# Kernel tuning notes

Measured on AMD Instinct MI355X. Metric: run time of the kernel, lower is better.

Reference implementation:

```python
import jax, jax.numpy as jnp
import numpy as np

B, L, N, D, C, WS, NH = 32, 64, 1024, 512, 8192, 3, 16
HD = D // NH          # head_dim = 32
HID = 2 * D           # MLP expansion = 2


def _ln(x, g, b, eps=1e-5):
    m = jnp.mean(x, -1, keepdims=True)
    v = jnp.mean((x - m) ** 2, -1, keepdims=True)
    return (x - m) * jax.lax.rsqrt(v + eps) * g + b


def setup_inputs() -> dict:
    key = jax.random.key(0)
    ks = jax.random.split(key, 16)
    r = lambda i, shape, s=0.02: jax.random.normal(ks[i], shape, jnp.float32) * s
    return dict(
        visual_features=jax.random.normal(ks[0], (B, N, D), jnp.float32),
        targets=jax.random.randint(ks[1], (B, L), 0, C),
        pad_id=1,
        char_embed=r(2, (C, D), 1.0),
        ln1_g=jnp.ones(D), ln1_b=jnp.zeros(D),
        in_proj_w=r(3, (3 * D, D)), in_proj_b=jnp.zeros(3 * D),
        out_w=r(4, (D, D)), out_b=jnp.zeros(D),
        fc1_w=r(5, (HID, D)), fc1_b=jnp.zeros(HID),
        fc2_w=r(6, (D, HID)), fc2_b=jnp.zeros(D),
        ln2_g=jnp.ones(D), ln2_b=jnp.zeros(D),
        left_token=r(7, (1, 1, D)), right_token=r(8, (1, 1, D)),
        q_w=r(9, (D, D)), q_b=jnp.zeros(D),
        kv_w=r(10, (2 * D, D)), kv_b=jnp.zeros(2 * D),
        proj_w=r(11, (D, D)), proj_b=jnp.zeros(D),
        lnq_g=jnp.ones(D), lnq_b=jnp.zeros(D),
        lnkv_g=jnp.ones(D), lnkv_b=jnp.zeros(D),
        head_w=r(12, (C, D)), head_b=jnp.zeros(C),
    )


def reference(visual_features, targets, pad_id, char_embed, ln1_g, ln1_b,
              in_proj_w, in_proj_b, out_w, out_b, fc1_w, fc1_b, fc2_w, fc2_b,
              ln2_g, ln2_b, left_token, right_token, q_w, q_b, kv_w, kv_b,
              proj_w, proj_b, lnq_g, lnq_b, lnkv_g, lnkv_b, head_w, head_b):
    # --- build left/right context windows via gather (vectorizes the python loop) ---
    padded = jnp.pad(targets, ((0, 0), (WS, WS)), constant_values=pad_id)
    li = jnp.arange(L)[:, None] + jnp.arange(WS)[None, :]      # (L, WS)
    left_ids = padded[:, li]                                   # (B, L, WS)
    right_ids = padded[:, li + WS + 1]                         # (B, L, WS)

    def encode(ids, tok):
        x = char_embed[ids] + tok                 # (B, L, WS, D)
        x = x.reshape(B * L, WS, D)               # (M, WS, D)
        xn = _ln(x, ln1_g, ln1_b)
        qkv = xn @ in_proj_w.T + in_proj_b
        q, k, v = jnp.split(qkv, 3, -1)
        sh = lambda t: t.reshape(B * L, WS, NH, HD).transpose(0, 2, 1, 3)
        q, k, v = sh(q), sh(k), sh(v)
        a = jax.nn.softmax(jnp.einsum('mhqd,mhkd->mhqk', q, k) * HD ** -0.5, -1)
        o = jnp.einsum('mhqk,mhkd->mhqd', a, v).transpose(0, 2, 1, 3).reshape(B * L, WS, D)
        x = x + o @ out_w.T + out_b
        h = jax.nn.gelu(_ln(x, ln2_g, ln2_b) @ fc1_w.T + fc1_b, approximate=False)
        x = x + h @ fc2_w.T + fc2_b
        return x.mean(1).reshape(B, L, D)

    def cross(qs):
        q = _ln(qs, lnq_g, lnq_b) @ q_w.T + q_b
        kv = _ln(visual_features, lnkv_g, lnkv_b) @ kv_w.T + kv_b
        k, v = jnp.split(kv, 2, -1)
        q = q.reshape(B, L, NH, HD).transpose(0, 2, 1, 3)
        k = k.reshape(B, N, NH, HD).transpose(0, 2, 1, 3)
        v = v.reshape(B, N, NH, HD).transpose(0, 2, 1, 3)
        a = jax.nn.softmax(jnp.einsum('bhld,bhnd->bhln', q, k) * HD ** -0.5, -1)
        o = jnp.einsum('bhln,bhnd->bhld', a, v).transpose(0, 2, 1, 3).reshape(B, L, D)
        return o @ proj_w.T + proj_b

    left_enc = encode(left_ids, left_token)
    right_enc = encode(right_ids, right_token)
    left_feat = left_enc + cross(left_enc)
    right_feat = right_enc + cross(right_enc)
    sgm_left = left_feat @ head_w.T + head_b      # (B, L, C)
    sgm_right = right_feat @ head_w.T + head_b    # (B, L, C)
    return sgm_left, sgm_right, targets
```

## Files before the change

### kernel.cpp

```cpp
#include <hip/hip_runtime.h>
#include <hip/hip_bf16.h>
#include <cstdint>
#include <cstddef>


typedef __attribute__((ext_vector_type(8))) short s16x8;
typedef __attribute__((ext_vector_type(8))) unsigned short u16x8;
typedef __attribute__((ext_vector_type(4))) unsigned short u16x4;
typedef __attribute__((ext_vector_type(4))) float f32x4;

__device__ __forceinline__ float b2f(unsigned short u) {
  union { unsigned int i; float f; } c; c.i = ((unsigned int)u) << 16; return c.f;
}
__device__ __forceinline__ unsigned short f2b(float f) {
  union { float f; unsigned int i; } c; c.f = f;
  unsigned int x = c.i;
  return (unsigned short)((x + 0x7FFFu + ((x >> 16) & 1u)) >> 16);
}

#define GLOAD16(gp, lp)                                                        \
  __builtin_amdgcn_global_load_lds(                                           \
      (const __attribute__((address_space(1))) void*)(gp),                    \
      (__attribute__((address_space(3))) void*)(lp), 16, 0, 0)

__global__ void cvt_f32_bf16(const float* __restrict__ s, unsigned short* __restrict__ d, int n4) {
  int i = blockIdx.x * 256 + threadIdx.x;
  if (i >= n4) return;
  float4 v = ((const float4*)s)[i];
  u16x4 o; o[0] = f2b(v.x); o[1] = f2b(v.y); o[2] = f2b(v.z); o[3] = f2b(v.w);
  *(u16x4*)(d + (size_t)i * 4) = o;
}

__global__ void embed_k(const int* __restrict__ targets, const int* __restrict__ pad_p,
                        const float* __restrict__ ce, const float* __restrict__ ltok,
                        const float* __restrict__ rtok, float* __restrict__ x) {
  int idx = blockIdx.x * 256 + threadIdx.x;
  if (idx >= 12288 * 128) return;
  int row = idx >> 7, d4 = idx & 127;
  int side = row >= 6144;
  int rem = row - side * 6144;
  int pos = rem / 3, w = rem - pos * 3;
  int b = pos >> 6, l = pos & 63;
  int id;
  if (!side) { int ti = l + w - 3; id = (ti >= 0) ? targets[(b << 6) + ti] : *pad_p; }
  else       { int ti = l + w + 1; id = (ti < 64) ? targets[(b << 6) + ti] : *pad_p; }
  float4 cv = ((const float4*)ce)[(size_t)id * 128 + d4];
  float4 tv = ((const float4*)(side ? rtok : ltok))[d4];
  float4 o; o.x = cv.x + tv.x; o.y = cv.y + tv.y; o.z = cv.z + tv.z; o.w = cv.w + tv.w;
  ((float4*)x)[idx] = o;
}

__global__ __launch_bounds__(256) void ln_rows(const float* __restrict__ in,
    const float* __restrict__ g, const float* __restrict__ b,
    unsigned short* __restrict__ out, int M) {
  int row = blockIdx.x * 4 + (threadIdx.x >> 6);
  int lane = threadIdx.x & 63;
  const float* rp = in + (size_t)row * 512;
  float4 v0 = ((const float4*)rp)[lane * 2];
  float4 v1 = ((const float4*)rp)[lane * 2 + 1];
  float vv[8] = {v0.x, v0.y, v0.z, v0.w, v1.x, v1.y, v1.z, v1.w};
  float s = 0.f, ss = 0.f;
#pragma unroll
  for (int j = 0; j < 8; ++j) { s += vv[j]; ss += vv[j] * vv[j]; }
#pragma unroll
  for (int o = 1; o < 64; o <<= 1) { s += __shfl_xor(s, o); ss += __shfl_xor(ss, o); }
  float mean = s * (1.0f / 512.0f);
  float var = ss * (1.0f / 512.0f) - mean * mean;
  float inv = rsqrtf(var + 1e-5f);
  int c = lane * 8;
  u16x8 o8;
#pragma unroll
  for (int j = 0; j < 8; ++j) o8[j] = f2b((vv[j] - mean) * inv * g[c + j] + b[c + j]);
  *(u16x8*)(out + (size_t)row * 512 + c) = o8;
}

template<int RES, int GELU, int OUTBF, int KVT>
__global__ __launch_bounds__(256) void gemm128(
    const unsigned short* __restrict__ A, const unsigned short* __restrict__ Bt,
    const float* __restrict__ bias, const float* __restrict__ res,
    void* __restrict__ outp, int M, int N, int K) {
  __shared__ unsigned short sA[2][8192];
  __shared__ unsigned short sB[2][8192];
  const int tid = threadIdx.x;
  const int nbx = gridDim.x;
  int id = blockIdx.y * nbx + blockIdx.x;
  {
    const int nwg = nbx * gridDim.y;
    if ((nwg & 7) == 0) id = (id & 7) * (nwg >> 3) + (id >> 3);
  }
  const int bm = (id / nbx) * 128, bn = (id % nbx) * 128;
  const int wave = tid >> 6, lane = tid & 63;
  const int wr = (wave >> 1) * 64, wc = (wave & 1) * 64;
  const int lrow = lane & 15, g = lane >> 4;
  f32x4 acc[4][4] = {};
  const int xoff = (((((lrow & 1) << 2) | g) ^ ((lrow >> 1) & 7)) << 3);
  const int baseA = ((wr >> 1) + (lrow >> 1)) * 64 + xoff;
  const int baseB = ((wc >> 1) + (lrow >> 1)) * 64 + xoff;
  const int slot8 = (tid & 7) ^ ((tid >> 3) & 7);
  const int srow = ((tid >> 3) << 1) + (slot8 >> 2);
  const int scol = (slot8 & 3) << 3;
  const unsigned short* gA = A + (size_t)(bm + srow) * K + scol;
  const unsigned short* gB = Bt + (size_t)(bn + srow) * K + scol;
  const int NT = K >> 6;

#define STAGE128(buf, kt)                                                      \
  { _Pragma("unroll")                                                          \
    for (int h = 0; h < 2; ++h) {                                              \
      _Pragma("unroll")                                                        \
      for (int i = 0; i < 2; ++i) {                                            \
        GLOAD16(gA + (size_t)(i * 64) * K + (kt) * 64 + h * 32,                \
                &sA[buf][h * 4096 + i * 2048 + wave * 512]);                   \
        GLOAD16(gB + (size_t)(i * 64) * K + (kt) * 64 + h * 32,                \
                &sB[buf][h * 4096 + i * 2048 + wave * 512]);                   \
      }                                                                        \
    } }

  STAGE128(0, 0);
  __syncthreads();
  int cur = 0;
  for (int kt = 0; kt < NT; ++kt) {
    s16x8 a0[4], b0[4];
#pragma unroll
    for (int m = 0; m < 4; ++m) a0[m] = *(const s16x8*)&sA[cur][baseA + m * 512];
#pragma unroll
    for (int n = 0; n < 4; ++n) b0[n] = *(const s16x8*)&sB[cur][baseB + n * 512];
    if (kt + 1 < NT) STAGE128(cur ^ 1, kt + 1);
    __builtin_amdgcn_s_setprio(1);
#pragma unroll
    for (int m = 0; m < 4; ++m)
#pragma unroll
      for (int n = 0; n < 4; ++n)
        acc[m][n] = __builtin_amdgcn_mfma_f32_16x16x32_bf16(b0[n], a0[m], acc[m][n], 0, 0, 0);
    __builtin_amdgcn_s_setprio(0);
    s16x8 a1[4], b1[4];
#pragma unroll
    for (int m = 0; m < 4; ++m) a1[m] = *(const s16x8*)&sA[cur][4096 + baseA + m * 512];
#pragma unroll
    for (int n = 0; n < 4; ++n) b1[n] = *(const s16x8*)&sB[cur][4096 + baseB + n * 512];
    __builtin_amdgcn_s_setprio(1);
#pragma unroll
    for (int m = 0; m < 4; ++m)
#pragma unroll
      for (int n = 0; n < 4; ++n)
        acc[m][n] = __builtin_amdgcn_mfma_f32_16x16x32_bf16(b1[n], a1[m], acc[m][n], 0, 0, 0);
    __builtin_amdgcn_s_setprio(0);
    __syncthreads();
    cur ^= 1;
  }
#undef STAGE128

  const int orow_ = bm + wr + lrow;
  const int ocol_ = bn + wc + g * 4;
#pragma unroll
  for (int m = 0; m < 4; ++m) {
    const int row = orow_ + m * 16;
#pragma unroll
    for (int n = 0; n < 4; ++n) {
      const int col = ocol_ + n * 16;
      f32x4 v = acc[m][n];
      f32x4 b4 = *(const f32x4*)(bias + col);
      v += b4;
      if (GELU) {
#pragma unroll
        for (int r = 0; r < 4; ++r)
          v[r] = 0.5f * v[r] * (1.0f + erff(v[r] * 0.70710678118654752f));
      }
      if (RES) v += *(const f32x4*)(res + (size_t)row * N + col);
      if (KVT) {
        int bb = row >> 10, nn = row & 1023;
        unsigned short* Kp = (unsigned short*)outp;
        unsigned short* VpT = Kp + 16777216u;
        if (col < 512) {
          int hh = col >> 5, dd = col & 31;
          u16x4 o4;
#pragma unroll
          for (int r = 0; r < 4; ++r) o4[r] = f2b(v[r]);
          *(u16x4*)(Kp + (((size_t)(bb * 16 + hh)) * 1024 + nn) * 32 + dd) = o4;
        } else {
          int cc = col - 512, hh = cc >> 5, dd = cc & 31;
#pragma unroll
          for (int r = 0; r < 4; ++r)
            VpT[(((size_t)(bb * 16 + hh)) * 32 + dd + r) * 1024 + nn] = f2b(v[r]);
        }
      } else if (OUTBF) {
        u16x4 o4;
#pragma unroll
        for (int r = 0; r < 4; ++r) o4[r] = f2b(v[r]);
        *(u16x4*)((unsigned short*)outp + (size_t)row * N + col) = o4;
      } else {
        *(f32x4*)((float*)outp + (size_t)row * N + col) = v;
      }
    }
  }
}

__global__ __launch_bounds__(256) void winattn(const unsigned short* __restrict__ qkv,
                                               unsigned short* __restrict__ o) {
  int g = blockIdx.x * 256 + threadIdx.x;
  if (g >= 4096 * 48) return;
  int i = g % 3;
  int t = g / 3;
  int h = t & 15;
  int sp = t >> 4;
  const unsigned short* base = qkv + (size_t)sp * 4608 + h * 32;
  float qv[32];
  {
    const u16x8* qp = (const u16x8*)(base + (size_t)i * 1536);
#pragma unroll
    for (int c = 0; c < 4; ++c) {
      u16x8 v = qp[c];
#pragma unroll
      for (int j = 0; j < 8; ++j) qv[c * 8 + j] = b2f(v[j]);
    }
  }
  float s[3];
#pragma unroll
  for (int j3 = 0; j3 < 3; ++j3) {
    const u16x8* kp = (const u16x8*)(base + (size_t)j3 * 1536 + 512);
    float acc = 0.f;
#pragma unroll
    for (int c = 0; c < 4; ++c) {
      u16x8 v = kp[c];
#pragma unroll
      for (int j = 0; j < 8; ++j) acc += qv[c * 8 + j] * b2f(v[j]);
    }
    s[j3] = acc * 0.17677669529663687f;
  }
  float mx = fmaxf(s[0], fmaxf(s[1], s[2]));
  float e0 = __expf(s[0] - mx), e1 = __expf(s[1] - mx), e2 = __expf(s[2] - mx);
  float inv = 1.0f / (e0 + e1 + e2);
  float a0 = e0 * inv, a1 = e1 * inv, a2 = e2 * inv;
  unsigned short* op = o + (size_t)(sp * 3 + i) * 512 + h * 32;
  const u16x8* v0p = (const u16x8*)(base + 1024);
  const u16x8* v1p = (const u16x8*)(base + 1536 + 1024);
  const u16x8* v2p = (const u16x8*)(base + 3072 + 1024);
#pragma unroll
  for (int c = 0; c < 4; ++c) {
    u16x8 x0 = v0p[c], x1 = v1p[c], x2 = v2p[c];
    u16x8 ov;
#pragma unroll
    for (int j = 0; j < 8; ++j)
      ov[j] = f2b(a0 * b2f(x0[j]) + a1 * b2f(x1[j]) + a2 * b2f(x2[j]));
    *(u16x8*)(op + c * 8) = ov;
  }
}

__global__ void mean3(const float* __restrict__ x, float* __restrict__ enc) {
  int i = blockIdx.x * 256 + threadIdx.x;
  if (i >= 4096 * 128) return;
  int p = i >> 7, d4 = i & 127;
  const float4* xp = (const float4*)x;
  float4 a = xp[(size_t)(p * 3 + 0) * 128 + d4];
  float4 b = xp[(size_t)(p * 3 + 1) * 128 + d4];
  float4 c = xp[(size_t)(p * 3 + 2) * 128 + d4];
  float4 o;
  o.x = (a.x + b.x + c.x) * (1.0f / 3.0f);
  o.y = (a.y + b.y + c.y) * (1.0f / 3.0f);
  o.z = (a.z + b.z + c.z) * (1.0f / 3.0f);
  o.w = (a.w + b.w + c.w) * (1.0f / 3.0f);
  ((float4*)enc)[i] = o;
}

__global__ __launch_bounds__(256) void crossattn_mfma(const float* __restrict__ q,
    const unsigned short* __restrict__ Kp, const unsigned short* __restrict__ VpT,
    unsigned short* __restrict__ o) {
  __shared__ unsigned short Plds[4][2][16 * 40];
  const int sbh = blockIdx.x;
  const int side = sbh >> 9, b = (sbh >> 4) & 31, h = sbh & 15;
  const int tid = threadIdx.x;
  const int w = tid >> 6, lane = tid & 63;
  const int ql = lane & 15, g = lane >> 4;
  const int qrow = side * 2048 + b * 64 + w * 16 + ql;
  const float SC = 0.17677669529663687f;
  s16x8 qf;
  {
    const float* qp = q + (size_t)qrow * 512 + h * 32 + g * 8;
    float4 qa = ((const float4*)qp)[0];
    float4 qb4 = ((const float4*)qp)[1];
    qf[0] = (short)f2b(qa.x * SC); qf[1] = (short)f2b(qa.y * SC);
    qf[2] = (short)f2b(qa.z * SC); qf[3] = (short)f2b(qa.w * SC);
    qf[4] = (short)f2b(qb4.x * SC); qf[5] = (short)f2b(qb4.y * SC);
    qf[6] = (short)f2b(qb4.z * SC); qf[7] = (short)f2b(qb4.w * SC);
  }
  const unsigned short* kbase = Kp + ((size_t)(b * 16 + h) * 1024) * 32;
  const unsigned short* vbase = VpT + ((size_t)(b * 16 + h) * 32) * 1024;
  f32x4 oacc0 = {}, oacc1 = {};
  float m_run = -1e30f, l_part = 0.f;
  for (int kv0 = 0; kv0 < 1024; kv0 += 32) {
    const int pp = (kv0 >> 5) & 1;
    s16x8 kf0 = *(const s16x8*)(kbase + (size_t)(kv0 + ql) * 32 + g * 8);
    s16x8 kf1 = *(const s16x8*)(kbase + (size_t)(kv0 + 16 + ql) * 32 + g * 8);
    f32x4 z = {0.f, 0.f, 0.f, 0.f};
    f32x4 s0 = __builtin_amdgcn_mfma_f32_16x16x32_bf16(kf0, qf, z, 0, 0, 0);
    f32x4 s1 = __builtin_amdgcn_mfma_f32_16x16x32_bf16(kf1, qf, z, 0, 0, 0);
    float cm = fmaxf(fmaxf(fmaxf(s0[0], s0[1]), fmaxf(s0[2], s0[3])),
                     fmaxf(fmaxf(s1[0], s1[1]), fmaxf(s1[2], s1[3])));
    cm = fmaxf(cm, __shfl_xor(cm, 16));
    cm = fmaxf(cm, __shfl_xor(cm, 32));
    float m_new = fmaxf(m_run, cm);
    float corr = __expf(m_run - m_new);
    m_run = m_new;
    float p0[4], p1[4], ps = 0.f;
#pragma unroll
    for (int r = 0; r < 4; ++r) {
      p0[r] = __expf(s0[r] - m_new);
      p1[r] = __expf(s1[r] - m_new);
      ps += p0[r] + p1[r];
    }
    l_part = l_part * corr + ps;
    oacc0 *= corr; oacc1 *= corr;
    u16x4 w0, w1;
#pragma unroll
    for (int r = 0; r < 4; ++r) { w0[r] = f2b(p0[r]); w1[r] = f2b(p1[r]); }
    *(u16x4*)&Plds[w][pp][ql * 40 + g * 4] = w0;
    *(u16x4*)&Plds[w][pp][ql * 40 + 16 + g * 4] = w1;
    __syncthreads();
    s16x8 pf = *(const s16x8*)&Plds[w][pp][ql * 40 + g * 8];
    s16x8 vf0 = *(const s16x8*)(vbase + (size_t)ql * 1024 + kv0 + g * 8);
    s16x8 vf1 = *(const s16x8*)(vbase + (size_t)(16 + ql) * 1024 + kv0 + g * 8);
    oacc0 = __builtin_amdgcn_mfma_f32_16x16x32_bf16(vf0, pf, oacc0, 0, 0, 0);
    oacc1 = __builtin_amdgcn_mfma_f32_16x16x32_bf16(vf1, pf, oacc1, 0, 0, 0);
  }
  float lf = l_part;
  lf += __shfl_xor(lf, 16);
  lf += __shfl_xor(lf, 32);
  float inv = 1.0f / lf;
  unsigned short* op = o + (size_t)qrow * 512 + h * 32;
  u16x4 ov0, ov1;
#pragma unroll
  for (int r = 0; r < 4; ++r) {
    ov0[r] = f2b(oacc0[r] * inv);
    ov1[r] = f2b(oacc1[r] * inv);
  }
  *(u16x4*)(op + g * 4) = ov0;
  *(u16x4*)(op + 16 + g * 4) = ov1;
}

__global__ void tail_targets(const int* __restrict__ t, float* __restrict__ out) {
  int i = blockIdx.x * 256 + threadIdx.x;
  if (i < 2048) out[33554432 + i] = (float)t[i];
}

extern "C" void kernel_launch(void* const* d_in, const int* in_sizes, int n_in,
                              void* d_out, int out_size, void* d_ws, size_t ws_size,
                              hipStream_t stream) {
  const float* visual   = (const float*)d_in[0];
  const int*   targets  = (const int*)d_in[1];
  const int*   pad_p    = (const int*)d_in[2];
  const float* char_emb = (const float*)d_in[3];
  const float* ln1_g = (const float*)d_in[4];
  const float* ln1_b = (const float*)d_in[5];
  const float* in_proj_w = (const float*)d_in[6];
  const float* in_proj_b = (const float*)d_in[7];
  const float* out_w = (const float*)d_in[8];
  const float* out_b = (const float*)d_in[9];
  const float* fc1_w = (const float*)d_in[10];
  const float* fc1_b = (const float*)d_in[11];
  const float* fc2_w = (const float*)d_in[12];
  const float* fc2_b = (const float*)d_in[13];
  const float* ln2_g = (const float*)d_in[14];
  const float* ln2_b = (const float*)d_in[15];
  const float* ltok  = (const float*)d_in[16];
  const float* rtok  = (const float*)d_in[17];
  const float* q_w   = (const float*)d_in[18];
  const float* q_b   = (const float*)d_in[19];
  const float* kv_w  = (const float*)d_in[20];
  const float* kv_b  = (const float*)d_in[21];
  const float* proj_w = (const float*)d_in[22];
  const float* proj_b = (const float*)d_in[23];
  const float* lnq_g = (const float*)d_in[24];
  const float* lnq_b = (const float*)d_in[25];
  const float* lnkv_g = (const float*)d_in[26];
  const float* lnkv_b = (const float*)d_in[27];
  const float* head_w = (const float*)d_in[28];
  const float* head_b = (const float*)d_in[29];

  char* ws = (char*)d_ws;
  unsigned short* W    = (unsigned short*)ws;
  float*          X    = (float*)(ws + 14680064ull);
  unsigned short* KP   = (unsigned short*)(ws + 14680064ull);
  unsigned short* A1   = (unsigned short*)(ws + 39845888ull);
  unsigned short* B1   = (unsigned short*)(ws + 52428800ull);
  unsigned short* QKV  = (unsigned short*)(ws + 77594624ull);
  float*          ENC  = (float*)(ws + 115343360ull);
  unsigned short* VIS  = (unsigned short*)(ws + 123731968ull);
  float*          Q    = (float*)(ws + 157286400ull);
  unsigned short* OC   = (unsigned short*)(ws + 165675008ull);
  unsigned short* FEAT = (unsigned short*)(ws + 169869312ull);
  unsigned short* LNQ  = (unsigned short*)(ws + 174063616ull);
  unsigned short* VPT  = KP + 16777216u;

  unsigned short* Wip   = W;
  unsigned short* Wout  = W + 786432;
  unsigned short* Wfc1  = W + 1048576;
  unsigned short* Wfc2  = W + 1572864;
  unsigned short* Wq    = W + 2097152;
  unsigned short* Wkv   = W + 2359296;
  unsigned short* Wproj = W + 2883584;
  unsigned short* Whead = W + 3145728;

  auto cvt = [&](const float* s, unsigned short* d, int n) {
    cvt_f32_bf16<<<dim3((n / 4 + 255) / 256), dim3(256), 0, stream>>>(s, d, n / 4);
  };
  cvt(in_proj_w, Wip, 786432);
  cvt(out_w, Wout, 262144);
  cvt(fc1_w, Wfc1, 524288);
  cvt(fc2_w, Wfc2, 524288);
  cvt(q_w, Wq, 262144);
  cvt(kv_w, Wkv, 524288);
  cvt(proj_w, Wproj, 262144);
  cvt(head_w, Whead, 4194304);

  embed_k<<<dim3(6144), dim3(256), 0, stream>>>(targets, pad_p, char_emb, ltok, rtok, X);
  ln_rows<<<dim3(3072), dim3(256), 0, stream>>>(X, ln1_g, ln1_b, A1, 12288);
  gemm128<0,0,1,0><<<dim3(12, 96), dim3(256), 0, stream>>>(A1, Wip, in_proj_b, nullptr, QKV, 12288, 1536, 512);
  winattn<<<dim3(768), dim3(256), 0, stream>>>(QKV, B1);
  gemm128<1,0,0,0><<<dim3(4, 96), dim3(256), 0, stream>>>(B1, Wout, out_b, X, X, 12288, 512, 512);
  ln_rows<<<dim3(3072), dim3(256), 0, stream>>>(X, ln2_g, ln2_b, A1, 12288);
  gemm128<0,1,1,0><<<dim3(8, 96), dim3(256), 0, stream>>>(A1, Wfc1, fc1_b, nullptr, B1, 12288, 1024, 512);
  gemm128<1,0,0,0><<<dim3(4, 96), dim3(256), 0, stream>>>(B1, Wfc2, fc2_b, X, X, 12288, 512, 1024);
  mean3<<<dim3(2048), dim3(256), 0, stream>>>(X, ENC);

  ln_rows<<<dim3(8192), dim3(256), 0, stream>>>(visual, lnkv_g, lnkv_b, VIS, 32768);
  gemm128<0,0,1,1><<<dim3(8, 256), dim3(256), 0, stream>>>(VIS, Wkv, kv_b, nullptr, KP, 32768, 1024, 512);
  ln_rows<<<dim3(1024), dim3(256), 0, stream>>>(ENC, lnq_g, lnq_b, LNQ, 4096);
  gemm128<0,0,0,0><<<dim3(4, 32), dim3(256), 0, stream>>>(LNQ, Wq, q_b, nullptr, Q, 4096, 512, 512);
  crossattn_mfma<<<dim3(1024), dim3(256), 0, stream>>>(Q, KP, VPT, OC);
  gemm128<1,0,1,0><<<dim3(4, 32), dim3(256), 0, stream>>>(OC, Wproj, proj_b, ENC, FEAT, 4096, 512, 512);

  gemm128<0,0,0,0><<<dim3(64, 32), dim3(256), 0, stream>>>(FEAT, Whead, head_b, nullptr, (float*)d_out, 4096, 8192, 512);
  tail_targets<<<dim3(8), dim3(256), 0, stream>>>(targets, (float*)d_out);
}
```

Before: 404.0 us.

## Store encoder residual stream and Q projection in bf16, remap GEMM tile order

The encoder residual stream X moves from fp32 to bf16. The embed, layernorm, residual-GEMM epilogue and mean kernels now read and write bf16, which halves their memory traffic. The Q projection output is also stored in bf16, and the cross-attention kernel reads it directly. The GEMM block-to-tile mapping now walks M first when the grid is wider than it is tall, which affects L2 reuse for the large head GEMM. Accumulating the residual in bf16 loses precision across the two residual additions.

```diff
diff --git a/kernel.cpp b/kernel.cpp
--- a/kernel.cpp
+++ b/kernel.cpp
@@ -33,7 +33,7 @@
 
 __global__ void embed_k(const int* __restrict__ targets, const int* __restrict__ pad_p,
                         const float* __restrict__ ce, const float* __restrict__ ltok,
-                        const float* __restrict__ rtok, float* __restrict__ x) {
+                        const float* __restrict__ rtok, unsigned short* __restrict__ x) {
   int idx = blockIdx.x * 256 + threadIdx.x;
   if (idx >= 12288 * 128) return;
   int row = idx >> 7, d4 = idx & 127;
@@ -46,19 +46,29 @@
   else       { int ti = l + w + 1; id = (ti < 64) ? targets[(b << 6) + ti] : *pad_p; }
   float4 cv = ((const float4*)ce)[(size_t)id * 128 + d4];
   float4 tv = ((const float4*)(side ? rtok : ltok))[d4];
-  float4 o; o.x = cv.x + tv.x; o.y = cv.y + tv.y; o.z = cv.z + tv.z; o.w = cv.w + tv.w;
-  ((float4*)x)[idx] = o;
-}
-
-__global__ __launch_bounds__(256) void ln_rows(const float* __restrict__ in,
+  u16x4 o; o[0] = f2b(cv.x + tv.x); o[1] = f2b(cv.y + tv.y);
+  o[2] = f2b(cv.z + tv.z); o[3] = f2b(cv.w + tv.w);
+  *(u16x4*)(x + (size_t)idx * 4) = o;
+}
+
+template<int INBF>
+__global__ __launch_bounds__(256) void ln_rows(const void* __restrict__ in,
     const float* __restrict__ g, const float* __restrict__ b,
     unsigned short* __restrict__ out, int M) {
   int row = blockIdx.x * 4 + (threadIdx.x >> 6);
   int lane = threadIdx.x & 63;
-  const float* rp = in + (size_t)row * 512;
-  float4 v0 = ((const float4*)rp)[lane * 2];
-  float4 v1 = ((const float4*)rp)[lane * 2 + 1];
-  float vv[8] = {v0.x, v0.y, v0.z, v0.w, v1.x, v1.y, v1.z, v1.w};
+  float vv[8];
+  if (INBF) {
+    u16x8 v8 = *(const u16x8*)((const unsigned short*)in + (size_t)row * 512 + lane * 8);
+#pragma unroll
+    for (int j = 0; j < 8; ++j) vv[j] = b2f(v8[j]);
+  } else {
+    const float* rp = (const float*)in + (size_t)row * 512;
+    float4 v0 = ((const float4*)rp)[lane * 2];
+    float4 v1 = ((const float4*)rp)[lane * 2 + 1];
+    vv[0] = v0.x; vv[1] = v0.y; vv[2] = v0.z; vv[3] = v0.w;
+    vv[4] = v1.x; vv[5] = v1.y; vv[6] = v1.z; vv[7] = v1.w;
+  }
   float s = 0.f, ss = 0.f;
 #pragma unroll
   for (int j = 0; j < 8; ++j) { s += vv[j]; ss += vv[j] * vv[j]; }
@@ -77,18 +87,20 @@
 template<int RES, int GELU, int OUTBF, int KVT>
 __global__ __launch_bounds__(256) void gemm128(
     const unsigned short* __restrict__ A, const unsigned short* __restrict__ Bt,
-    const float* __restrict__ bias, const float* __restrict__ res,
+    const float* __restrict__ bias, const void* __restrict__ res,
     void* __restrict__ outp, int M, int N, int K) {
   __shared__ unsigned short sA[2][8192];
   __shared__ unsigned short sB[2][8192];
   const int tid = threadIdx.x;
-  const int nbx = gridDim.x;
+  const int nbx = gridDim.x, nby = gridDim.y;
   int id = blockIdx.y * nbx + blockIdx.x;
   {
-    const int nwg = nbx * gridDim.y;
+    const int nwg = nbx * nby;
     if ((nwg & 7) == 0) id = (id & 7) * (nwg >> 3) + (id >> 3);
   }
-  const int bm = (id / nbx) * 128, bn = (id % nbx) * 128;
+  int bm, bn;
+  if (nbx >= nby) { bm = (id % nby) * 128; bn = (id / nby) * 128; }
+  else            { bm = (id / nbx) * 128; bn = (id % nbx) * 128; }
   const int wave = tid >> 6, lane = tid & 63;
   const int wr = (wave >> 1) * 64, wc = (wave & 1) * 64;
   const int lrow = lane & 15, g = lane >> 4;
@@ -165,7 +177,12 @@
         for (int r = 0; r < 4; ++r)
           v[r] = 0.5f * v[r] * (1.0f + erff(v[r] * 0.70710678118654752f));
       }
-      if (RES) v += *(const f32x4*)(res + (size_t)row * N + col);
+      if (RES == 1) v += *(const f32x4*)((const float*)res + (size_t)row * N + col);
+      if (RES == 2) {
+        u16x4 r4 = *(const u16x4*)((const unsigned short*)res + (size_t)row * N + col);
+#pragma unroll
+        for (int r = 0; r < 4; ++r) v[r] += b2f(r4[r]);
+      }
       if (KVT) {
         int bb = row >> 10, nn = row & 1023;
         unsigned short* Kp = (unsigned short*)outp;
@@ -245,23 +262,22 @@
   }
 }
 
-__global__ void mean3(const float* __restrict__ x, float* __restrict__ enc) {
+__global__ void mean3(const unsigned short* __restrict__ x, float* __restrict__ enc) {
   int i = blockIdx.x * 256 + threadIdx.x;
   if (i >= 4096 * 128) return;
   int p = i >> 7, d4 = i & 127;
-  const float4* xp = (const float4*)x;
-  float4 a = xp[(size_t)(p * 3 + 0) * 128 + d4];
-  float4 b = xp[(size_t)(p * 3 + 1) * 128 + d4];
-  float4 c = xp[(size_t)(p * 3 + 2) * 128 + d4];
+  u16x4 a = *(const u16x4*)(x + ((size_t)(p * 3 + 0) * 512 + d4 * 4));
+  u16x4 b = *(const u16x4*)(x + ((size_t)(p * 3 + 1) * 512 + d4 * 4));
+  u16x4 c = *(const u16x4*)(x + ((size_t)(p * 3 + 2) * 512 + d4 * 4));
   float4 o;
-  o.x = (a.x + b.x + c.x) * (1.0f / 3.0f);
-  o.y = (a.y + b.y + c.y) * (1.0f / 3.0f);
-  o.z = (a.z + b.z + c.z) * (1.0f / 3.0f);
-  o.w = (a.w + b.w + c.w) * (1.0f / 3.0f);
+  o.x = (b2f(a[0]) + b2f(b[0]) + b2f(c[0])) * (1.0f / 3.0f);
+  o.y = (b2f(a[1]) + b2f(b[1]) + b2f(c[1])) * (1.0f / 3.0f);
+  o.z = (b2f(a[2]) + b2f(b[2]) + b2f(c[2])) * (1.0f / 3.0f);
+  o.w = (b2f(a[3]) + b2f(b[3]) + b2f(c[3])) * (1.0f / 3.0f);
   ((float4*)enc)[i] = o;
 }
 
-__global__ __launch_bounds__(256) void crossattn_mfma(const float* __restrict__ q,
+__global__ __launch_bounds__(256) void crossattn_mfma(const unsigned short* __restrict__ q,
     const unsigned short* __restrict__ Kp, const unsigned short* __restrict__ VpT,
     unsigned short* __restrict__ o) {
   __shared__ unsigned short Plds[4][2][16 * 40];
@@ -274,13 +290,9 @@
   const float SC = 0.17677669529663687f;
   s16x8 qf;
   {
-    const float* qp = q + (size_t)qrow * 512 + h * 32 + g * 8;
-    float4 qa = ((const float4*)qp)[0];
-    float4 qb4 = ((const float4*)qp)[1];
-    qf[0] = (short)f2b(qa.x * SC); qf[1] = (short)f2b(qa.y * SC);
-    qf[2] = (short)f2b(qa.z * SC); qf[3] = (short)f2b(qa.w * SC);
-    qf[4] = (short)f2b(qb4.x * SC); qf[5] = (short)f2b(qb4.y * SC);
-    qf[6] = (short)f2b(qb4.z * SC); qf[7] = (short)f2b(qb4.w * SC);
+    u16x8 qv8 = *(const u16x8*)(q + (size_t)qrow * 512 + h * 32 + g * 8);
+#pragma unroll
+    for (int j = 0; j < 8; ++j) qf[j] = (short)f2b(b2f(qv8[j]) * SC);
   }
   const unsigned short* kbase = Kp + ((size_t)(b * 16 + h) * 1024) * 32;
   const unsigned short* vbase = VpT + ((size_t)(b * 16 + h) * 32) * 1024;
@@ -377,14 +389,14 @@
 
   char* ws = (char*)d_ws;
   unsigned short* W    = (unsigned short*)ws;
-  float*          X    = (float*)(ws + 14680064ull);
+  unsigned short* XB   = (unsigned short*)(ws + 14680064ull);
   unsigned short* KP   = (unsigned short*)(ws + 14680064ull);
   unsigned short* A1   = (unsigned short*)(ws + 39845888ull);
   unsigned short* B1   = (unsigned short*)(ws + 52428800ull);
   unsigned short* QKV  = (unsigned short*)(ws + 77594624ull);
   float*          ENC  = (float*)(ws + 115343360ull);
   unsigned short* VIS  = (unsigned short*)(ws + 123731968ull);
-  float*          Q    = (float*)(ws + 157286400ull);
+  unsigned short* Q    = (unsigned short*)(ws + 157286400ull);
   unsigned short* OC   = (unsigned short*)(ws + 165675008ull);
   unsigned short* FEAT = (unsigned short*)(ws + 169869312ull);
   unsigned short* LNQ  = (unsigned short*)(ws + 174063616ull);
@@ -411,20 +423,20 @@
   cvt(proj_w, Wproj, 262144);
   cvt(head_w, Whead, 4194304);
 
-  embed_k<<<dim3(6144), dim3(256), 0, stream>>>(targets, pad_p, char_emb, ltok, rtok, X);
-  ln_rows<<<dim3(3072), dim3(256), 0, stream>>>(X, ln1_g, ln1_b, A1, 12288);
+  embed_k<<<dim3(6144), dim3(256), 0, stream>>>(targets, pad_p, char_emb, ltok, rtok, XB);
+  ln_rows<1><<<dim3(3072), dim3(256), 0, stream>>>(XB, ln1_g, ln1_b, A1, 12288);
   gemm128<0,0,1,0><<<dim3(12, 96), dim3(256), 0, stream>>>(A1, Wip, in_proj_b, nullptr, QKV, 12288, 1536, 512);
   winattn<<<dim3(768), dim3(256), 0, stream>>>(QKV, B1);
-  gemm128<1,0,0,0><<<dim3(4, 96), dim3(256), 0, stream>>>(B1, Wout, out_b, X, X, 12288, 512, 512);
-  ln_rows<<<dim3(3072), dim3(256), 0, stream>>>(X, ln2_g, ln2_b, A1, 12288);
+  gemm128<2,0,1,0><<<dim3(4, 96), dim3(256), 0, stream>>>(B1, Wout, out_b, XB, XB, 12288, 512, 512);
+  ln_rows<1><<<dim3(3072), dim3(256), 0, stream>>>(XB, ln2_g, ln2_b, A1, 12288);
   gemm128<0,1,1,0><<<dim3(8, 96), dim3(256), 0, stream>>>(A1, Wfc1, fc1_b, nullptr, B1, 12288, 1024, 512);
-  gemm128<1,0,0,0><<<dim3(4, 96), dim3(256), 0, stream>>>(B1, Wfc2, fc2_b, X, X, 12288, 512, 1024);
-  mean3<<<dim3(2048), dim3(256), 0, stream>>>(X, ENC);
-
-  ln_rows<<<dim3(8192), dim3(256), 0, stream>>>(visual, lnkv_g, lnkv_b, VIS, 32768);
+  gemm128<2,0,1,0><<<dim3(4, 96), dim3(256), 0, stream>>>(B1, Wfc2, fc2_b, XB, XB, 12288, 512, 1024);
+  mean3<<<dim3(2048), dim3(256), 0, stream>>>(XB, ENC);
+
+  ln_rows<0><<<dim3(8192), dim3(256), 0, stream>>>(visual, lnkv_g, lnkv_b, VIS, 32768);
   gemm128<0,0,1,1><<<dim3(8, 256), dim3(256), 0, stream>>>(VIS, Wkv, kv_b, nullptr, KP, 32768, 1024, 512);
-  ln_rows<<<dim3(1024), dim3(256), 0, stream>>>(ENC, lnq_g, lnq_b, LNQ, 4096);
-  gemm128<0,0,0,0><<<dim3(4, 32), dim3(256), 0, stream>>>(LNQ, Wq, q_b, nullptr, Q, 4096, 512, 512);
+  ln_rows<0><<<dim3(1024), dim3(256), 0, stream>>>(ENC, lnq_g, lnq_b, LNQ, 4096);
+  gemm128<0,0,1,0><<<dim3(4, 32), dim3(256), 0, stream>>>(LNQ, Wq, q_b, nullptr, Q, 4096, 512, 512);
   crossattn_mfma<<<dim3(1024), dim3(256), 0, stream>>>(Q, KP, VPT, OC);
   gemm128<1,0,1,0><<<dim3(4, 32), dim3(256), 0, stream>>>(OC, Wproj, proj_b, ENC, FEAT, 4096, 512, 512);
 
```

After: 416.9 us. 3.2% more time.
